# Optimization experiments

Measured on AMD Instinct MI355X. Metric: run time of the kernel, lower is better.

The kernel has to match this reference:

```python
import jax, jax.numpy as jnp
import numpy as np

N_NODES = 100000
N_EDGES = 1600000
IN_C, HID_C, OUT_C = 128, 128, 64


def setup_inputs() -> dict:
    key = jax.random.key(0)
    ks = jax.random.split(key, 9)
    features = jax.random.normal(ks[0], (N_NODES, IN_C), dtype=jnp.float32)
    src = jax.random.randint(ks[1], (N_EDGES,), 0, N_NODES, dtype=jnp.int32)
    dst = jax.random.randint(ks[2], (N_EDGES,), 0, N_NODES, dtype=jnp.int32)
    def glorot(k, fan_in, fan_out):
        lim = float(np.sqrt(6.0 / (fan_in + fan_out)))
        return jax.random.uniform(k, (fan_in, fan_out), jnp.float32, -lim, lim)
    return {
        "features": features, "src": src, "dst": dst,
        "W1": glorot(ks[3], IN_C, HID_C), "b1": jnp.zeros((HID_C,), jnp.float32),
        "W2": glorot(ks[4], HID_C, HID_C), "b2": jnp.zeros((HID_C,), jnp.float32),
        "W3": glorot(ks[5], HID_C, OUT_C), "b3": jnp.zeros((OUT_C,), jnp.float32),
    }


def _graph_conv(x, src, dst, W, b, inv_sqrt_out, inv_sqrt_in):
    # DGL GraphConv, norm='both': h = D_in^{-1/2} A D_out^{-1/2} (x W) + b
    h = (x * inv_sqrt_out[:, None]) @ W            # [N, out]
    agg = jax.ops.segment_sum(h[src], dst, num_segments=N_NODES)
    return agg * inv_sqrt_in[:, None] + b


def reference(features, src, dst, W1, b1, W2, b2, W3, b3):
    ones = jnp.ones((N_EDGES,), jnp.float32)
    deg_out = jnp.clip(jax.ops.segment_sum(ones, src, num_segments=N_NODES), 1.0)
    deg_in = jnp.clip(jax.ops.segment_sum(ones, dst, num_segments=N_NODES), 1.0)
    iso, isi = deg_out ** -0.5, deg_in ** -0.5
    x = jax.nn.relu(_graph_conv(features, src, dst, W1, b1, iso, isi))
    x = jax.nn.relu(_graph_conv(x, src, dst, W2, b2, iso, isi))
    x = _graph_conv(x, src, dst, W3, b3, iso, isi)
    return jax.nn.log_softmax(x, axis=1)
```

## Files before the change

kernel.cpp:

```cpp
#include <hip/hip_runtime.h>
#include <hip/hip_bf16.h>

#define IN_C 128
#define HID_C 128
#define OUT_C 64

typedef unsigned short u16;
typedef unsigned int   u32;
typedef __attribute__((ext_vector_type(8))) short short8;
typedef __attribute__((ext_vector_type(4))) float f32x4;
typedef __attribute__((ext_vector_type(2))) float f32x2;

__device__ __forceinline__ u16 bf16_bits(float x) {
    __hip_bfloat16 h = __float2bfloat16(x);
    return *(u16*)&h;
}
__device__ __forceinline__ void split_hi_lo(float a, u16& hi, u16& lo) {
    __hip_bfloat16 h = __float2bfloat16(a);
    float hf = __bfloat162float(h);
    __hip_bfloat16 l = __float2bfloat16(a - hf);
    hi = *(u16*)&h; lo = *(u16*)&l;
}
__device__ __forceinline__ void pk_acc(f32x2& acc, u32 v) {
    f32x2 val;
    val.x = __uint_as_float(v << 16);
    val.y = __uint_as_float(v & 0xffff0000u);
    asm("v_pk_add_f32 %0, %0, %1" : "+v"(acc) : "v"(val));
}


__global__ __launch_bounds__(256)
void part_hist(const int* __restrict__ keys, int* __restrict__ bh,
               int E, int K, int NB) {
    const int b = blockIdx.x;
    extern __shared__ int lh[];
    for (int i = threadIdx.x; i < K; i += 256) lh[i] = 0;
    __syncthreads();
    const int lo = (int)((long long)E * b / NB);
    const int hi = (int)((long long)E * (b + 1) / NB);
    for (int i = lo + threadIdx.x; i < hi; i += 256)
        atomicAdd(&lh[keys[i] >> 8], 1);
    __syncthreads();
    for (int k = threadIdx.x; k < K; k += 256)
        bh[k * NB + b] = lh[k];
}

template <bool PACK>
__global__ __launch_bounds__(256)
void part_scatter(const int* __restrict__ keys, const int* __restrict__ other,
                  const int* __restrict__ ofs, u32* __restrict__ out,
                  int E, int K, int NB) {
    const int b = blockIdx.x;
    extern __shared__ int lcur[];
    for (int k = threadIdx.x; k < K; k += 256) lcur[k] = ofs[k * NB + b];
    __syncthreads();
    const int lo = (int)((long long)E * b / NB);
    const int hi = (int)((long long)E * (b + 1) / NB);
    for (int i = lo + threadIdx.x; i < hi; i += 256) {
        int key = keys[i];
        int p = atomicAdd(&lcur[key >> 8], 1);
        out[p] = PACK ? (((u32)other[i] << 8) | (u32)(key & 255)) : (u32)key;
    }
}

__global__ __launch_bounds__(256)
void bucket_count(const u32* __restrict__ pairs, const int* __restrict__ ofs,
                  int* __restrict__ cnt, int N, int NB, int K, int cap) {
    const int k = blockIdx.x;
    __shared__ int lc[256];
    lc[threadIdx.x] = 0;
    __syncthreads();
    const int s0 = ofs[k * NB];
    const int s1 = (k == K - 1) ? cap : ofs[(k + 1) * NB];
    for (int i = s0 + threadIdx.x; i < s1; i += 256)
        atomicAdd(&lc[pairs[i] & 255], 1);
    __syncthreads();
    const int node = k * 256 + threadIdx.x;
    if (node < N) cnt[node] = lc[threadIdx.x];
}

__global__ __launch_bounds__(256)
void bucket_fill(const u32* __restrict__ pairs, const int* __restrict__ ofs,
                 const int* __restrict__ row_start, int* __restrict__ csr,
                 int N, int NB, int K, int E) {
    const int k = blockIdx.x;
    __shared__ int lcur[256];
    const int node = k * 256 + threadIdx.x;
    lcur[threadIdx.x] = (node < N) ? row_start[node] : 0;
    __syncthreads();
    const int s0 = ofs[k * NB];
    const int s1 = (k == K - 1) ? E : ofs[(k + 1) * NB];
    for (int i = s0 + threadIdx.x; i < s1; i += 256) {
        u32 pr = pairs[i];
        int p = atomicAdd(&lcur[pr & 255], 1);
        csr[p] = (int)(pr >> 8);
    }
}


__global__ __launch_bounds__(256)
void scan_pass1(const int* __restrict__ in, int* __restrict__ blocksum, int M) {
    const int b = blockIdx.x, t = threadIdx.x;
    const int base = b * 1024 + t * 4;
    int s = 0;
#pragma unroll
    for (int j = 0; j < 4; ++j) {
        int idx = base + j;
        if (idx < M) s += in[idx];
    }
#pragma unroll
    for (int off = 32; off >= 1; off >>= 1) s += __shfl_xor(s, off);
    __shared__ int wsum[4];
    if ((t & 63) == 0) wsum[t >> 6] = s;
    __syncthreads();
    if (t == 0) blocksum[b] = wsum[0] + wsum[1] + wsum[2] + wsum[3];
}

__global__ __launch_bounds__(1024)
void scan_g2(int* __restrict__ a, int nb) {
    __shared__ int s[1024];
    const int t = threadIdx.x;
    int v = (t < nb) ? a[t] : 0;
    s[t] = v;
    __syncthreads();
    for (int off = 1; off < 1024; off <<= 1) {
        int x = (t >= off) ? s[t - off] : 0;
        __syncthreads();
        s[t] += x;
        __syncthreads();
    }
    if (t < nb) a[t] = s[t] - v;
}

__global__ __launch_bounds__(256)
void scan_g3(const int* __restrict__ in, const int* __restrict__ blockoff,
             int* __restrict__ out, int M) {
    __shared__ int ssum[256];
    const int b = blockIdx.x, t = threadIdx.x;
    const int base = b * 1024 + t * 4;
    int c[4];
#pragma unroll
    for (int j = 0; j < 4; ++j) {
        int idx = base + j;
        c[j] = (idx < M) ? in[idx] : 0;
    }
    const int tot = c[0] + c[1] + c[2] + c[3];
    ssum[t] = tot;
    __syncthreads();
    for (int off = 1; off < 256; off <<= 1) {
        int v = (t >= off) ? ssum[t - off] : 0;
        __syncthreads();
        ssum[t] += v;
        __syncthreads();
    }
    int run = blockoff[b] + ssum[t] - tot;
#pragma unroll
    for (int j = 0; j < 4; ++j) {
        int idx = base + j;
        if (idx < M) { out[idx] = run; run += c[j]; }
    }
}

__global__ __launch_bounds__(256)
void scan_pass3n(const int* __restrict__ cnt_in, const int* __restrict__ cnt_out,
                 const int* __restrict__ blockoff, int* __restrict__ row_start,
                 float* __restrict__ iso, float* __restrict__ isi, int N, int E) {
    __shared__ int ssum[256];
    const int b = blockIdx.x, t = threadIdx.x;
    const int base = b * 1024 + t * 4;
    int c[4];
#pragma unroll
    for (int j = 0; j < 4; ++j) {
        int idx = base + j;
        c[j] = (idx < N) ? cnt_in[idx] : 0;
    }
    const int tot = c[0] + c[1] + c[2] + c[3];
    ssum[t] = tot;
    __syncthreads();
    for (int off = 1; off < 256; off <<= 1) {
        int v = (t >= off) ? ssum[t - off] : 0;
        __syncthreads();
        ssum[t] += v;
        __syncthreads();
    }
    int run = blockoff[b] + ssum[t] - tot;
#pragma unroll
    for (int j = 0; j < 4; ++j) {
        int idx = base + j;
        if (idx < N) {
            row_start[idx] = run;
            run += c[j];
            int di = c[j] < 1 ? 1 : c[j];
            int co = cnt_out[idx];
            int dd = co < 1 ? 1 : co;
            isi[idx] = rsqrtf((float)di);
            iso[idx] = rsqrtf((float)dd);
        }
    }
    if (b == 0 && t == 0) row_start[N] = E;
}


__global__ __launch_bounds__(128)
void wt_prep_all(const float* __restrict__ W1, const float* __restrict__ W2,
                 const float* __restrict__ W3, u16* __restrict__ Wt1,
                 u16* __restrict__ Wt2, u16* __restrict__ Wt3) {
    const int b = blockIdx.x, k = threadIdx.x;
    if (b < 128)       Wt1[b * 128 + k] = bf16_bits(W1[k * 128 + b]);
    else if (b < 256)  { int c = b - 128; Wt2[c * 128 + k] = bf16_bits(W2[k * 128 + c]); }
    else               { int c = b - 256; Wt3[c * 128 + k] = bf16_bits(W3[k * 64 + c]); }
}

template <int C>
__device__ __forceinline__
void mfma_store(const u16* sAh, const u16* sAl, const u16* __restrict__ Wt,
                u16* __restrict__ H, int row0, int N, int t) {
    constexpr int NT = C / 16;
    const int wid = t >> 6, lane = t & 63;
    const int r0 = wid * 16;
    const int arow = r0 + (lane & 15);
    const int kb = (lane >> 4) * 8;

    f32x4 acc[NT];
#pragma unroll
    for (int i = 0; i < NT; ++i) acc[i] = (f32x4){0.f, 0.f, 0.f, 0.f};

    const u16* wbase = Wt + (size_t)(lane & 15) * 128 + kb;

#pragma unroll
    for (int kk = 0; kk < 4; ++kk) {
        short8 ah = *(const short8*)(&sAh[arow * 136 + kk * 32 + kb]);
        short8 al = *(const short8*)(&sAl[arow * 136 + kk * 32 + kb]);
#pragma unroll
        for (int ct = 0; ct < NT; ++ct) {
            short8 bf = *(const short8*)(wbase + ct * 16 * 128 + kk * 32);
            acc[ct] = __builtin_amdgcn_mfma_f32_16x16x32_bf16(ah, bf, acc[ct], 0, 0, 0);
            acc[ct] = __builtin_amdgcn_mfma_f32_16x16x32_bf16(al, bf, acc[ct], 0, 0, 0);
        }
    }

    const int rbase = row0 + r0 + (lane >> 4) * 4;
#pragma unroll
    for (int ct = 0; ct < NT; ++ct) {
        int gcol = ct * 16 + (lane & 15);
#pragma unroll
        for (int r = 0; r < 4; ++r) {
            int grow = rbase + r;
            if (grow < N) H[(size_t)grow * C + gcol] = bf16_bits(acc[ct][r]);
        }
    }
}


__device__ __forceinline__
f32x2 gather128(const u16* __restrict__ Hin, const int* __restrict__ csr_src,
                int rs, int re, int lane) {
    f32x2 acc; acc.x = 0.f; acc.y = 0.f;
    int e = rs;
    while (e < re) {
        int nloc = re - e;
        if (nloc > 64) nloc = 64;
        int idx = (lane < nloc) ? csr_src[e + lane] : 0;
        int j = 0;
        for (; j + 8 <= nloc; j += 8) {
            u32 v[8];
#pragma unroll
            for (int q = 0; q < 8; ++q) {
                int s = __builtin_amdgcn_readlane(idx, j + q);
                v[q] = *(const u32*)(Hin + (size_t)s * 128 + lane * 2);
            }
#pragma unroll
            for (int q = 0; q < 8; ++q) pk_acc(acc, v[q]);
        }
        for (; j + 4 <= nloc; j += 4) {
            u32 v[4];
#pragma unroll
            for (int q = 0; q < 4; ++q) {
                int s = __builtin_amdgcn_readlane(idx, j + q);
                v[q] = *(const u32*)(Hin + (size_t)s * 128 + lane * 2);
            }
#pragma unroll
            for (int q = 0; q < 4; ++q) pk_acc(acc, v[q]);
        }
        for (; j < nloc; ++j) {
            int s = __builtin_amdgcn_readlane(idx, j);
            pk_acc(acc, *(const u32*)(Hin + (size_t)s * 128 + lane * 2));
        }
        e += nloc;
    }
    return acc;
}


__global__ __launch_bounds__(256)
void gemm1_fused(const float* __restrict__ X, const float* __restrict__ iso,
                 const u16* __restrict__ Wt, u16* __restrict__ H, int N) {
    __shared__ u16 sAh[64 * 136];
    __shared__ u16 sAl[64 * 136];
    const int t = threadIdx.x;
    const int row0 = blockIdx.x * 64;

    for (int i = t; i < 2048; i += 256) {
        int r = i >> 5, kv = (i & 31) << 2;
        int gr = row0 + r;
        if (gr >= N) gr = N - 1;
        float s = iso[gr];
        float4 x = *(const float4*)(X + (size_t)gr * 128 + kv);
        u16 h0, l0, h1, l1, h2, l2, h3, l3;
        split_hi_lo(x.x * s, h0, l0);
        split_hi_lo(x.y * s, h1, l1);
        split_hi_lo(x.z * s, h2, l2);
        split_hi_lo(x.w * s, h3, l3);
        uint2 hp = make_uint2((u32)h0 | ((u32)h1 << 16), (u32)h2 | ((u32)h3 << 16));
        uint2 lp = make_uint2((u32)l0 | ((u32)l1 << 16), (u32)l2 | ((u32)l3 << 16));
        *(uint2*)(&sAh[r * 136 + kv]) = hp;
        *(uint2*)(&sAl[r * 136 + kv]) = lp;
    }
    __syncthreads();
    mfma_store<128>(sAh, sAl, Wt, H, row0, N, t);
}


template <int C>
__global__ __launch_bounds__(256)
void agg_gemm(const u16* __restrict__ Hin, const int* __restrict__ row_start,
              const int* __restrict__ csr_src, const float* __restrict__ isi,
              const float* __restrict__ iso, const float* __restrict__ bias,
              const u16* __restrict__ Wt, u16* __restrict__ Hout, int N) {
    __shared__ u16 sAh[64 * 136];
    __shared__ u16 sAl[64 * 136];
    const int t = threadIdx.x, wid = t >> 6, lane = t & 63;
    const int row0 = blockIdx.x * 64;
    const float2 b2 = *(const float2*)(bias + lane * 2);

    for (int i = 0; i < 16; ++i) {
        int r = wid * 16 + i;
        int n = row0 + r;
        if (n < N) {
            int rs = row_start[n], re = row_start[n + 1];
            f32x2 acc = gather128(Hin, csr_src, rs, re, lane);
            float sc = isi[n], so = iso[n];
            float o0 = fmaxf(acc.x * sc + b2.x, 0.f) * so;
            float o1 = fmaxf(acc.y * sc + b2.y, 0.f) * so;
            u16 h0, l0, h1, l1;
            split_hi_lo(o0, h0, l0);
            split_hi_lo(o1, h1, l1);
            *(u32*)(&sAh[r * 136 + lane * 2]) = (u32)h0 | ((u32)h1 << 16);
            *(u32*)(&sAl[r * 136 + lane * 2]) = (u32)l0 | ((u32)l1 << 16);
        }
    }
    __syncthreads();
    mfma_store<C>(sAh, sAl, Wt, Hout, row0, N, t);
}


__global__ __launch_bounds__(256)
void agg_final(const u16* __restrict__ H, const int* __restrict__ row_start,
               const int* __restrict__ csr_src, const float* __restrict__ isi,
               const float* __restrict__ bias, float* __restrict__ Out, int N) {
    const int wid  = (int)((blockIdx.x * (size_t)blockDim.x + threadIdx.x) >> 6);
    const int lane = threadIdx.x & 63;
    if (wid >= N) return;
    const int rs = row_start[wid];
    const int re = row_start[wid + 1];
    const float sc = isi[wid];

    float a = 0.f;
    int e = rs;
    while (e < re) {
        int nloc = re - e;
        if (nloc > 64) nloc = 64;
        int idx = (lane < nloc) ? csr_src[e + lane] : 0;
        int j = 0;
        for (; j + 8 <= nloc; j += 8) {
            u32 v[8];
#pragma unroll
            for (int q = 0; q < 8; ++q) {
                int s = __builtin_amdgcn_readlane(idx, j + q);
                v[q] = H[(size_t)s * 64 + lane];
            }
#pragma unroll
            for (int q = 0; q < 8; ++q) a += __uint_as_float(v[q] << 16);
        }
        for (; j + 4 <= nloc; j += 4) {
            u32 v[4];
#pragma unroll
            for (int q = 0; q < 4; ++q) {
                int s = __builtin_amdgcn_readlane(idx, j + q);
                v[q] = H[(size_t)s * 64 + lane];
            }
#pragma unroll
            for (int q = 0; q < 4; ++q) a += __uint_as_float(v[q] << 16);
        }
        for (; j < nloc; ++j) {
            int s = __builtin_amdgcn_readlane(idx, j);
            a += __uint_as_float((u32)H[(size_t)s * 64 + lane] << 16);
        }
        e += nloc;
    }
    float v = a * sc + bias[lane];
    float m = v;
#pragma unroll
    for (int off = 32; off >= 1; off >>= 1) m = fmaxf(m, __shfl_xor(m, off));
    float ex = expf(v - m);
    float ss = ex;
#pragma unroll
    for (int off = 32; off >= 1; off >>= 1) ss += __shfl_xor(ss, off);
    v = (v - m) - logf(ss);
    Out[(size_t)wid * 64 + lane] = v;
}


extern "C" void kernel_launch(void* const* d_in, const int* in_sizes, int n_in,
                              void* d_out, int out_size, void* d_ws, size_t ws_size,
                              hipStream_t stream) {
    const float* features = (const float*)d_in[0];
    const int*   src      = (const int*)d_in[1];
    const int*   dst      = (const int*)d_in[2];
    const float* W1       = (const float*)d_in[3];
    const float* b1       = (const float*)d_in[4];
    const float* W2       = (const float*)d_in[5];
    const float* b2       = (const float*)d_in[6];
    const float* W3       = (const float*)d_in[7];
    const float* b3       = (const float*)d_in[8];
    float*       out      = (float*)d_out;

    const int N  = in_sizes[0] / IN_C;
    const int E  = in_sizes[1];
    const int K  = (N + 255) >> 8;
    const int NB = 256;
    const int M  = 2 * K * NB;
    const int nbe = (M + 1023) / 1024;
    const int nb  = (N + 1023) / 1024;

    char* ws = (char*)d_ws;
    const size_t SLOT = 400128;
    int*   cnt_out   = (int*)(ws + 0 * SLOT);
    int*   cnt_in    = (int*)(ws + 1 * SLOT);
    int*   row_start = (int*)(ws + 2 * SLOT);
    float* iso       = (float*)(ws + 3 * SLOT);
    float* isi       = (float*)(ws + 4 * SLOT);
    int*   blocksum  = (int*)(ws + 5 * SLOT);
    int*   eblocksum = blocksum + 2048;
    int*   csr       = (int*)(ws + 6 * SLOT);
    char*  p         = ws + 6 * SLOT + 6400000;
    int*   BH        = (int*)p;
    int*   OFS       = (int*)(p + 1000000);
    u32*   pairs     = (u32*)(p + 2000000);
    u16*   Hb1       = (u16*)(p + 14800000);
    u16*   Hb2       = (u16*)(p + 40400000);
    u16*   Wt1       = (u16*)(p + 66000000);
    u16*   Wt2       = Wt1 + 128 * 128;
    u16*   Wt3       = Wt2 + 128 * 128;

    const size_t ldsK = (size_t)K * sizeof(int);

    part_hist<<<NB, 256, ldsK, stream>>>(dst, BH,           E, K, NB);
    part_hist<<<NB, 256, ldsK, stream>>>(src, BH + K * NB,  E, K, NB);
    scan_pass1<<<nbe, 256, 0, stream>>>(BH, eblocksum, M);
    scan_g2<<<1, 1024, 0, stream>>>(eblocksum, nbe);
    scan_g3<<<nbe, 256, 0, stream>>>(BH, eblocksum, OFS, M);
    part_scatter<true ><<<NB, 256, ldsK, stream>>>(dst, src, OFS,          pairs, E, K, NB);
    part_scatter<false><<<NB, 256, ldsK, stream>>>(src, src, OFS + K * NB, pairs, E, K, NB);
    bucket_count<<<K, 256, 0, stream>>>(pairs, OFS,          cnt_in,  N, NB, K, E);
    bucket_count<<<K, 256, 0, stream>>>(pairs, OFS + K * NB, cnt_out, N, NB, K, 2 * E);
    scan_pass1<<<nb, 256, 0, stream>>>(cnt_in, blocksum, N);
    scan_g2<<<1, 1024, 0, stream>>>(blocksum, nb);
    scan_pass3n<<<nb, 256, 0, stream>>>(cnt_in, cnt_out, blocksum, row_start, iso, isi, N, E);
    bucket_fill<<<K, 256, 0, stream>>>(pairs, OFS, row_start, csr, N, NB, K, E);

    wt_prep_all<<<320, 128, 0, stream>>>(W1, W2, W3, Wt1, Wt2, Wt3);

    const int gblocks = (N + 63) / 64;
    const int ablocks = (int)(((size_t)N * 64 + 255) / 256);

    gemm1_fused<<<gblocks, 256, 0, stream>>>(features, iso, Wt1, Hb1, N);
    agg_gemm<128><<<gblocks, 256, 0, stream>>>(Hb1, row_start, csr, isi, iso, b1, Wt2, Hb2, N);
    agg_gemm<64><<<gblocks, 256, 0, stream>>>(Hb2, row_start, csr, isi, iso, b2, Wt3, Hb1, N);
    agg_final<<<ablocks, 256, 0, stream>>>(Hb1, row_start, csr, isi, b3, out, N);
}
```

Measured before the change: 427.2 us.

## Split fused aggregate+GEMM into separate wave-per-node aggregation and MFMA GEMM kernels

The fused aggregate-then-GEMM kernels, where each block gathered 64 rows serially per wave before the MFMA step, are split in two. A wave-per-node aggregation kernel writes hi/lo bf16 activations to global memory, and a separate GEMM kernel loads them into LDS. The aim is better load balance and more parallelism in the irregular gather. The cost is an extra global round trip of the split activations plus extra kernel launches. The gather unroll also grows from 8 to 16 loads in flight.

```diff
diff --git a/kernel.cpp b/kernel.cpp
--- a/kernel.cpp
+++ b/kernel.cpp
@@ -249,46 +249,6 @@
             if (grow < N) H[(size_t)grow * C + gcol] = bf16_bits(acc[ct][r]);
         }
     }
-}
-
-
-__device__ __forceinline__
-f32x2 gather128(const u16* __restrict__ Hin, const int* __restrict__ csr_src,
-                int rs, int re, int lane) {
-    f32x2 acc; acc.x = 0.f; acc.y = 0.f;
-    int e = rs;
-    while (e < re) {
-        int nloc = re - e;
-        if (nloc > 64) nloc = 64;
-        int idx = (lane < nloc) ? csr_src[e + lane] : 0;
-        int j = 0;
-        for (; j + 8 <= nloc; j += 8) {
-            u32 v[8];
-#pragma unroll
-            for (int q = 0; q < 8; ++q) {
-                int s = __builtin_amdgcn_readlane(idx, j + q);
-                v[q] = *(const u32*)(Hin + (size_t)s * 128 + lane * 2);
-            }
-#pragma unroll
-            for (int q = 0; q < 8; ++q) pk_acc(acc, v[q]);
-        }
-        for (; j + 4 <= nloc; j += 4) {
-            u32 v[4];
-#pragma unroll
-            for (int q = 0; q < 4; ++q) {
-                int s = __builtin_amdgcn_readlane(idx, j + q);
-                v[q] = *(const u32*)(Hin + (size_t)s * 128 + lane * 2);
-            }
-#pragma unroll
-            for (int q = 0; q < 4; ++q) pk_acc(acc, v[q]);
-        }
-        for (; j < nloc; ++j) {
-            int s = __builtin_amdgcn_readlane(idx, j);
-            pk_acc(acc, *(const u32*)(Hin + (size_t)s * 128 + lane * 2));
-        }
-        e += nloc;
-    }
-    return acc;
 }
 
 
@@ -323,34 +283,87 @@
 
 template <int C>
 __global__ __launch_bounds__(256)
-void agg_gemm(const u16* __restrict__ Hin, const int* __restrict__ row_start,
+void gemm_mfma(const u16* __restrict__ Ah, const u16* __restrict__ Al,
+               const u16* __restrict__ Wt, u16* __restrict__ H, int N) {
+    __shared__ u16 sAh[64 * 136];
+    __shared__ u16 sAl[64 * 136];
+    const int t = threadIdx.x;
+    const int row0 = blockIdx.x * 64;
+
+    for (int c = t; c < 1024; c += 256) {
+        int r = c >> 4, kc = c & 15;
+        int gr = row0 + r;
+        if (gr >= N) gr = N - 1;
+        *(uint4*)(&sAh[r * 136 + kc * 8]) = *(const uint4*)(Ah + (size_t)gr * 128 + kc * 8);
+        *(uint4*)(&sAl[r * 136 + kc * 8]) = *(const uint4*)(Al + (size_t)gr * 128 + kc * 8);
+    }
+    __syncthreads();
+    mfma_store<C>(sAh, sAl, Wt, H, row0, N, t);
+}
+
+
+__device__ __forceinline__
+f32x2 gather128(const u16* __restrict__ Hin, const int* __restrict__ csr_src,
+                int rs, int re, int lane) {
+    f32x2 acc; acc.x = 0.f; acc.y = 0.f;
+    int e = rs;
+    while (e < re) {
+        int nloc = re - e;
+        if (nloc > 64) nloc = 64;
+        int idx = (lane < nloc) ? csr_src[e + lane] : 0;
+        int j = 0;
+        for (; j + 16 <= nloc; j += 16) {
+            u32 v[16];
+#pragma unroll
+            for (int q = 0; q < 16; ++q) {
+                int s = __builtin_amdgcn_readlane(idx, j + q);
+                v[q] = *(const u32*)(Hin + (size_t)s * 128 + lane * 2);
+            }
+#pragma unroll
+            for (int q = 0; q < 16; ++q) pk_acc(acc, v[q]);
+        }
+        for (; j + 4 <= nloc; j += 4) {
+            u32 v[4];
+#pragma unroll
+            for (int q = 0; q < 4; ++q) {
+                int s = __builtin_amdgcn_readlane(idx, j + q);
+                v[q] = *(const u32*)(Hin + (size_t)s * 128 + lane * 2);
+            }
+#pragma unroll
+            for (int q = 0; q < 4; ++q) pk_acc(acc, v[q]);
+        }
+        for (; j < nloc; ++j) {
+            int s = __builtin_amdgcn_readlane(idx, j);
+            pk_acc(acc, *(const u32*)(Hin + (size_t)s * 128 + lane * 2));
+        }
+        e += nloc;
+    }
+    return acc;
+}
+
+
+__global__ __launch_bounds__(256)
+void agg_relu(const u16* __restrict__ H, const int* __restrict__ row_start,
               const int* __restrict__ csr_src, const float* __restrict__ isi,
               const float* __restrict__ iso, const float* __restrict__ bias,
-              const u16* __restrict__ Wt, u16* __restrict__ Hout, int N) {
-    __shared__ u16 sAh[64 * 136];
-    __shared__ u16 sAl[64 * 136];
-    const int t = threadIdx.x, wid = t >> 6, lane = t & 63;
-    const int row0 = blockIdx.x * 64;
-    const float2 b2 = *(const float2*)(bias + lane * 2);
-
-    for (int i = 0; i < 16; ++i) {
-        int r = wid * 16 + i;
-        int n = row0 + r;
-        if (n < N) {
-            int rs = row_start[n], re = row_start[n + 1];
-            f32x2 acc = gather128(Hin, csr_src, rs, re, lane);
-            float sc = isi[n], so = iso[n];
-            float o0 = fmaxf(acc.x * sc + b2.x, 0.f) * so;
-            float o1 = fmaxf(acc.y * sc + b2.y, 0.f) * so;
-            u16 h0, l0, h1, l1;
-            split_hi_lo(o0, h0, l0);
-            split_hi_lo(o1, h1, l1);
-            *(u32*)(&sAh[r * 136 + lane * 2]) = (u32)h0 | ((u32)h1 << 16);
-            *(u32*)(&sAl[r * 136 + lane * 2]) = (u32)l0 | ((u32)l1 << 16);
-        }
-    }
-    __syncthreads();
-    mfma_store<C>(sAh, sAl, Wt, Hout, row0, N, t);
+              u16* __restrict__ Ah, u16* __restrict__ Al, int N) {
+    const int wid  = (int)((blockIdx.x * (size_t)blockDim.x + threadIdx.x) >> 6);
+    const int lane = threadIdx.x & 63;
+    if (wid >= N) return;
+    const int rs = row_start[wid];
+    const int re = row_start[wid + 1];
+
+    f32x2 acc = gather128(H, csr_src, rs, re, lane);
+
+    float2 b = *(const float2*)(bias + lane * 2);
+    const float sc = isi[wid], so = iso[wid];
+    float o0 = fmaxf(acc.x * sc + b.x, 0.f) * so;
+    float o1 = fmaxf(acc.y * sc + b.y, 0.f) * so;
+    u16 h0, l0, h1, l1;
+    split_hi_lo(o0, h0, l0);
+    split_hi_lo(o1, h1, l1);
+    ((u32*)Ah)[(size_t)wid * 64 + lane] = (u32)h0 | ((u32)h1 << 16);
+    ((u32*)Al)[(size_t)wid * 64 + lane] = (u32)l0 | ((u32)l1 << 16);
 }
 
 
@@ -447,9 +460,10 @@
     int*   BH        = (int*)p;
     int*   OFS       = (int*)(p + 1000000);
     u32*   pairs     = (u32*)(p + 2000000);
-    u16*   Hb1       = (u16*)(p + 14800000);
-    u16*   Hb2       = (u16*)(p + 40400000);
-    u16*   Wt1       = (u16*)(p + 66000000);
+    u16*   Hb        = (u16*)(p + 14800000);
+    u16*   Ah        = (u16*)(p + 40400000);
+    u16*   Al        = (u16*)(p + 66000000);
+    u16*   Wt1       = (u16*)(p + 91600000);
     u16*   Wt2       = Wt1 + 128 * 128;
     u16*   Wt3       = Wt2 + 128 * 128;
 
@@ -474,8 +488,10 @@
     const int gblocks = (N + 63) / 64;
     const int ablocks = (int)(((size_t)N * 64 + 255) / 256);
 
-    gemm1_fused<<<gblocks, 256, 0, stream>>>(features, iso, Wt1, Hb1, N);
-    agg_gemm<128><<<gblocks, 256, 0, stream>>>(Hb1, row_start, csr, isi, iso, b1, Wt2, Hb2, N);
-    agg_gemm<64><<<gblocks, 256, 0, stream>>>(Hb2, row_start, csr, isi, iso, b2, Wt3, Hb1, N);
-    agg_final<<<ablocks, 256, 0, stream>>>(Hb1, row_start, csr, isi, b3, out, N);
-}
+    gemm1_fused<<<gblocks, 256, 0, stream>>>(features, iso, Wt1, Hb, N);
+    agg_relu<<<ablocks, 256, 0, stream>>>(Hb, row_start, csr, isi, iso, b1, Ah, Al, N);
+    gemm_mfma<128><<<gblocks, 256, 0, stream>>>(Ah, Al, Wt2, Hb, N);
+    agg_relu<<<ablocks, 256, 0, stream>>>(Hb, row_start, csr, isi, iso, b2, Ah, Al, N);
+    gemm_mfma<64><<<gblocks, 256, 0, stream>>>(Ah, Al, Wt3, Hb, N);
+    agg_final<<<ablocks, 256, 0, stream>>>(Hb, row_start, csr, isi, b3, out, N);
+}
```

Result: faster. 373.0 us (-12.7%).
